# Performance work log

Measured on AMD Instinct MI355X. Metric: run time of the kernel, lower is better.

The kernel has to match this reference:

```python
import jax, jax.numpy as jnp
import numpy as np

B, N, NVT, HS, NZ = 512, 256, 32, 128, 64


def setup_inputs() -> dict:
    key = jax.random.key(0)
    ks = jax.random.split(key, 16)
    node_types = jax.random.randint(ks[0], (B, N), 0, NVT, dtype=jnp.int32)
    node_types = node_types.at[:, 0].set(0)      # START_TYPE
    node_types = node_types.at[:, -1].set(1)     # END_TYPE
    adj = jax.random.randint(ks[1], (B, N, N), 0, 2, dtype=jnp.int32)
    # DAG: edges only u -> v with u < v (strict upper triangular)
    tri = jnp.triu(jnp.ones((N, N), jnp.int32), k=1)
    adj = adj * tri[None, :, :]
    s = 0.05
    p = lambda k, shp: (jax.random.normal(k, shp, jnp.float32) * s)
    return {
        "node_types": node_types,
        "adj": adj,
        "W_ih": p(ks[2], (3 * HS, NVT)),   # grue_forward weight_ih
        "W_hh": p(ks[3], (3 * HS, HS)),    # grue_forward weight_hh
        "b_ih": p(ks[4], (3 * HS,)),
        "b_hh": p(ks[5], (3 * HS,)),
        "Wg": p(ks[6], (HS, NVT)),         # gate_forward linear
        "bg": p(ks[7], (HS,)),
        "Wm": p(ks[8], (HS, NVT)),         # mapper_forward (no bias)
        "W1": p(ks[9], (NZ, HS)),          # fc1 -> mu
        "b1": p(ks[10], (NZ,)),
        "W2": p(ks[11], (NZ, HS)),         # fc2 -> logvar
        "b2": p(ks[12], (NZ,)),
    }


def reference(node_types, adj, W_ih, W_hh, b_ih, b_hh, Wg, bg, Wm, W1, b1, W2, b2):
    hs = Wg.shape[0]
    # one-hot vertex types  [B, N, nvt]
    X = jax.nn.one_hot(node_types, Wg.shape[1], dtype=W_ih.dtype)
    # gated message from each vertex's TYPE (mapper has no bias -> padding contributes 0)
    gated = jax.nn.sigmoid(jnp.einsum('bnv,hv->bnh', X, Wg) + bg) \
            * jnp.einsum('bnv,hv->bnh', X, Wm)                      # [B, N, hs]
    A = adj.astype(gated.dtype)
    # predecessor aggregation: H_v = sum_{u: u->v} gated_u
    Hpre = jnp.einsum('buv,buh->bvh', A, gated)                     # [B, N, hs]
    # torch GRUCell(X_v, Hpre_v), vectorized over all vertices (no recurrence:
    # messages depend only on predecessor types)
    gi = jnp.einsum('bnv,gv->bng', X, W_ih) + b_ih                  # [B, N, 3hs]
    gh = jnp.einsum('bnh,gh->bng', Hpre, W_hh) + b_hh
    r = jax.nn.sigmoid(gi[..., :hs] + gh[..., :hs])
    z = jax.nn.sigmoid(gi[..., hs:2 * hs] + gh[..., hs:2 * hs])
    n = jnp.tanh(gi[..., 2 * hs:] + r * gh[..., 2 * hs:])
    Hv = (1.0 - z) * n + z * Hpre                                   # H_forward, [B, N, hs]
    # graph state: sum over vertices [1, N-1) (start=1, end_offset=1)
    Hg = Hv[:, 1:-1, :].sum(axis=1)                                 # [B, hs]
    mu = Hg @ W1.T + b1
    logvar = Hg @ W2.T + b2
    return (mu, logvar)
```

## Files before the change

### kernel.cpp

```cpp
#include <hip/hip_runtime.h>
#include <hip/hip_bf16.h>

#define HS 128
#define NVT 32
#define NN 256

typedef __attribute__((ext_vector_type(8))) short bf16x8;
typedef __attribute__((ext_vector_type(4))) float f32x4;

#define TABB_OFF 0
#define GIT_OFF  32768

static __device__ __forceinline__ short f2bs(float f) {
    __hip_bfloat16 h = __float2bfloat16(f);
    short s; __builtin_memcpy(&s, &h, 2);
    return s;
}
static __device__ __forceinline__ float bs2f(short s) {
    __hip_bfloat16 h; __builtin_memcpy(&h, &s, 2);
    return __bfloat162float(h);
}
static __device__ __forceinline__ float sigm(float x) {
    return __builtin_amdgcn_rcpf(1.f + __expf(-x));
}

__global__ void __launch_bounds__(512) build_tables(
    const float* __restrict__ W_ih, const float* __restrict__ W_hh,
    const float* __restrict__ b_ih, const float* __restrict__ b_hh,
    const float* __restrict__ Wg,   const float* __restrict__ bg,
    const float* __restrict__ Wm,
    short* __restrict__ TABB, short* __restrict__ GIT)
{
    __shared__ float G_s[HS];
    const int t = blockIdx.x;
    const int j = threadIdx.x;
    if (j < HS) {
        float x = Wg[j * NVT + t] + bg[j];
        G_s[j] = sigm(x) * Wm[j * NVT + t];
    }
    __syncthreads();
    if (j < 384) {
        float acc = 0.f;
        for (int h = 0; h < HS; ++h) acc += G_s[h] * W_hh[j * HS + h];
        TABB[j * NVT + t] = f2bs(acc);
        float git = W_ih[j * NVT + t] + b_ih[j];
        if (j < 256) git += b_hh[j];
        GIT[t * 384 + j] = f2bs(git);
    } else {
        TABB[j * NVT + t] = f2bs(G_s[j - 384]);
    }
}

__global__ void __launch_bounds__(256) dvae_fused(
    const int* __restrict__ node_types, const int* __restrict__ adj,
    const short* __restrict__ TABB, const short* __restrict__ GIT,
    const float* __restrict__ b_hh,
    const float* __restrict__ W1, const float* __restrict__ b1,
    const float* __restrict__ W2, const float* __restrict__ b2,
    float* __restrict__ out)
{
    __shared__ short cntA[NN * 40];
    __shared__ short GITs[NVT * 388];
    __shared__ int   types_s[NN];
    __shared__ float hgp[4 * HS];
    __shared__ float hg_s[HS];

    const int b = blockIdx.x, tid = threadIdx.x;
    const int wave = tid >> 6, lane = tid & 63;
    const int quad = lane >> 4, col = lane & 15;

    types_s[tid] = node_types[b * NN + tid];

    {
        const unsigned* src = (const unsigned*)GIT;
        unsigned* dst = (unsigned*)GITs;
        #pragma unroll
        for (int c = 0; c < 24; ++c) {
            int i = c * 256 + tid;
            int t = i / 192, j = i - t * 192;
            dst[t * 194 + j] = src[i];
        }
    }

    const int* adjb = adj + (size_t)b * NN * NN;
    const int v = tid;
    unsigned c0 = 0, c1 = 0, c2 = 0, c3 = 0, c4 = 0, c5 = 0, c6 = 0, c7 = 0;
    for (int u0 = 0; u0 < NN; u0 += 32) {
        int av[32];
        #pragma unroll
        for (int j = 0; j < 32; ++j) av[j] = adjb[(u0 + j) * NN + v];
        #pragma unroll
        for (int j = 0; j < 32; ++j) {
            unsigned t = (unsigned)__builtin_amdgcn_readfirstlane(types_s[u0 + j]);
            unsigned inc = ((unsigned)av[j]) << ((t & 3u) * 8u);
            switch (t >> 2) {
                case 0: c0 += inc; break;
                case 1: c1 += inc; break;
                case 2: c2 += inc; break;
                case 3: c3 += inc; break;
                case 4: c4 += inc; break;
                case 5: c5 += inc; break;
                case 6: c6 += inc; break;
                default: c7 += inc; break;
            }
        }
    }
    {
        unsigned cc[8] = {c0, c1, c2, c3, c4, c5, c6, c7};
        unsigned* dst = (unsigned*)cntA;
        #pragma unroll
        for (int k = 0; k < 8; ++k) {
            float f0 = (float)(cc[k] & 0xFF),         f1 = (float)((cc[k] >> 8) & 0xFF);
            float f2 = (float)((cc[k] >> 16) & 0xFF), f3 = (float)((cc[k] >> 24) & 0xFF);
            unsigned p0 = (unsigned)(unsigned short)f2bs(f0) | ((unsigned)(unsigned short)f2bs(f1) << 16);
            unsigned p1 = (unsigned)(unsigned short)f2bs(f2) | ((unsigned)(unsigned short)f2bs(f3) << 16);
            dst[v * 20 + 2 * k]     = p0;
            dst[v * 20 + 2 * k + 1] = p1;
        }
    }

    bf16x8 bfrag[8];
    #pragma unroll
    for (int i = 0; i < 8; ++i) {
        int gate = i >> 1, sub = (i & 1) * 16;
        int jb = (gate < 3 ? gate * 128 : 384) + wave * 32 + sub;
        bfrag[i] = *(const bf16x8*)(TABB + (jb + col) * 32 + quad * 8);
    }
    const int h0 = wave * 32 + col;
    const float bhn0 = b_hh[256 + h0], bhn1 = b_hh[256 + h0 + 16];
    float hg0 = 0.f, hg1 = 0.f;
    __syncthreads();

    for (int m = 0; m < 16; ++m) {
        bf16x8 afrag = *(const bf16x8*)(cntA + (m * 16 + col) * 40 + quad * 8);
        f32x4 acc[8];
        #pragma unroll
        for (int i = 0; i < 8; ++i)
            acc[i] = __builtin_amdgcn_mfma_f32_16x16x32_bf16(
                afrag, bfrag[i], (f32x4){0.f, 0.f, 0.f, 0.f}, 0, 0, 0);
        #pragma unroll
        for (int r = 0; r < 4; ++r) {
            int vv = m * 16 + quad * 4 + r;
            int tv = types_s[vv];
            float msk = (vv >= 1 && vv < NN - 1) ? 1.f : 0.f;
            const short* g = GITs + tv * 388;
            {
                float gir = bs2f(g[h0]), giz = bs2f(g[128 + h0]), gin = bs2f(g[256 + h0]);
                float rr = sigm(gir + acc[0][r]);
                float zz = sigm(giz + acc[2][r]);
                float x2 = gin + rr * (acc[4][r] + bhn0);
                float nt = 1.f - 2.f * __builtin_amdgcn_rcpf(1.f + __expf(2.f * x2));
                hg0 += msk * ((1.f - zz) * nt + zz * acc[6][r]);
            }
            {
                int h1 = h0 + 16;
                float gir = bs2f(g[h1]), giz = bs2f(g[128 + h1]), gin = bs2f(g[256 + h1]);
                float rr = sigm(gir + acc[1][r]);
                float zz = sigm(giz + acc[3][r]);
                float x2 = gin + rr * (acc[5][r] + bhn1);
                float nt = 1.f - 2.f * __builtin_amdgcn_rcpf(1.f + __expf(2.f * x2));
                hg1 += msk * ((1.f - zz) * nt + zz * acc[7][r]);
            }
        }
    }

    hgp[quad * HS + h0]      = hg0;
    hgp[quad * HS + h0 + 16] = hg1;
    __syncthreads();
    if (tid < HS)
        hg_s[tid] = (hgp[tid] + hgp[HS + tid]) + (hgp[2 * HS + tid] + hgp[3 * HS + tid]);
    __syncthreads();
    if (tid < 128) {
        int which = tid >> 6, zz = tid & 63;
        const float* W = which ? W2 : W1;
        float acc2 = which ? b2[zz] : b1[zz];
        #pragma unroll 4
        for (int h = 0; h < HS; ++h) acc2 += hg_s[h] * W[zz * HS + h];
        out[which * 32768 + b * 64 + zz] = acc2;
    }
}

extern "C" void kernel_launch(void* const* d_in, const int* in_sizes, int n_in,
                              void* d_out, int out_size, void* d_ws, size_t ws_size,
                              hipStream_t stream)
{
    const int* node_types = (const int*)d_in[0];
    const int* adj        = (const int*)d_in[1];
    const float* W_ih = (const float*)d_in[2];
    const float* W_hh = (const float*)d_in[3];
    const float* b_ih = (const float*)d_in[4];
    const float* b_hh = (const float*)d_in[5];
    const float* Wg   = (const float*)d_in[6];
    const float* bg   = (const float*)d_in[7];
    const float* Wm   = (const float*)d_in[8];
    const float* W1   = (const float*)d_in[9];
    const float* b1   = (const float*)d_in[10];
    const float* W2   = (const float*)d_in[11];
    const float* b2   = (const float*)d_in[12];

    char* ws = (char*)d_ws;
    short* TABB = (short*)(ws + TABB_OFF);
    short* GIT  = (short*)(ws + GIT_OFF);
    float* out  = (float*)d_out;

    build_tables<<<dim3(32), dim3(512), 0, stream>>>(W_ih, W_hh, b_ih, b_hh, Wg, bg, Wm, TABB, GIT);
    dvae_fused<<<dim3(512), dim3(256), 0, stream>>>(node_types, adj, TABB, GIT, b_hh, W1, b1, W2, b2, out);
}
```

Before: 247.8 us.

## Count predecessor types via adjacency bitmasks and popcount, double block to 512 threads

```diff
diff --git a/kernel.cpp b/kernel.cpp
--- a/kernel.cpp
+++ b/kernel.cpp
@@ -51,7 +51,7 @@
     }
 }
 
-__global__ void __launch_bounds__(256) dvae_fused(
+__global__ void __launch_bounds__(512) dvae_fused(
     const int* __restrict__ node_types, const int* __restrict__ adj,
     const short* __restrict__ TABB, const short* __restrict__ GIT,
     const float* __restrict__ b_hh,
@@ -59,123 +59,125 @@
     const float* __restrict__ W2, const float* __restrict__ b2,
     float* __restrict__ out)
 {
-    __shared__ short cntA[NN * 40];
+    __shared__ unsigned cntA[NN * 20];
     __shared__ short GITs[NVT * 388];
-    __shared__ int   types_s[NN];
-    __shared__ float hgp[4 * HS];
+    __shared__ unsigned tmask[NVT * 8];
+    __shared__ int types_s[NN];
     __shared__ float hg_s[HS];
 
     const int b = blockIdx.x, tid = threadIdx.x;
     const int wave = tid >> 6, lane = tid & 63;
     const int quad = lane >> 4, col = lane & 15;
 
-    types_s[tid] = node_types[b * NN + tid];
+    if (tid < NN) types_s[tid] = node_types[b * NN + tid];
 
     {
         const unsigned* src = (const unsigned*)GIT;
         unsigned* dst = (unsigned*)GITs;
         #pragma unroll
-        for (int c = 0; c < 24; ++c) {
-            int i = c * 256 + tid;
+        for (int c = 0; c < 12; ++c) {
+            int i = c * 512 + tid;
             int t = i / 192, j = i - t * 192;
             dst[t * 194 + j] = src[i];
         }
     }
 
-    const int* adjb = adj + (size_t)b * NN * NN;
-    const int v = tid;
-    unsigned c0 = 0, c1 = 0, c2 = 0, c3 = 0, c4 = 0, c5 = 0, c6 = 0, c7 = 0;
-    for (int u0 = 0; u0 < NN; u0 += 32) {
-        int av[32];
-        #pragma unroll
-        for (int j = 0; j < 32; ++j) av[j] = adjb[(u0 + j) * NN + v];
-        #pragma unroll
-        for (int j = 0; j < 32; ++j) {
-            unsigned t = (unsigned)__builtin_amdgcn_readfirstlane(types_s[u0 + j]);
-            unsigned inc = ((unsigned)av[j]) << ((t & 3u) * 8u);
-            switch (t >> 2) {
-                case 0: c0 += inc; break;
-                case 1: c1 += inc; break;
-                case 2: c2 += inc; break;
-                case 3: c3 += inc; break;
-                case 4: c4 += inc; break;
-                case 5: c5 += inc; break;
-                case 6: c6 += inc; break;
-                default: c7 += inc; break;
-            }
-        }
-    }
-    {
-        unsigned cc[8] = {c0, c1, c2, c3, c4, c5, c6, c7};
-        unsigned* dst = (unsigned*)cntA;
-        #pragma unroll
-        for (int k = 0; k < 8; ++k) {
-            float f0 = (float)(cc[k] & 0xFF),         f1 = (float)((cc[k] >> 8) & 0xFF);
-            float f2 = (float)((cc[k] >> 16) & 0xFF), f3 = (float)((cc[k] >> 24) & 0xFF);
-            unsigned p0 = (unsigned)(unsigned short)f2bs(f0) | ((unsigned)(unsigned short)f2bs(f1) << 16);
-            unsigned p1 = (unsigned)(unsigned short)f2bs(f2) | ((unsigned)(unsigned short)f2bs(f3) << 16);
-            dst[v * 20 + 2 * k]     = p0;
-            dst[v * 20 + 2 * k + 1] = p1;
-        }
-    }
-
-    bf16x8 bfrag[8];
+    bf16x8 bfrag[4];
     #pragma unroll
-    for (int i = 0; i < 8; ++i) {
-        int gate = i >> 1, sub = (i & 1) * 16;
-        int jb = (gate < 3 ? gate * 128 : 384) + wave * 32 + sub;
-        bfrag[i] = *(const bf16x8*)(TABB + (jb + col) * 32 + quad * 8);
-    }
-    const int h0 = wave * 32 + col;
-    const float bhn0 = b_hh[256 + h0], bhn1 = b_hh[256 + h0 + 16];
-    float hg0 = 0.f, hg1 = 0.f;
-    __syncthreads();
-
+    for (int g = 0; g < 4; ++g) {
+        int jb = (g < 3 ? g * 128 : 384) + wave * 16;
+        bfrag[g] = *(const bf16x8*)(TABB + (jb + col) * 32 + quad * 8);
+    }
+    const int h0 = wave * 16 + col;
+    const float bhn = b_hh[256 + h0];
+
+    unsigned cb[8];
+    if (tid < NN) {
+        const int* colp = adj + (size_t)b * NN * NN + tid;
+        #pragma unroll
+        for (int w8 = 0; w8 < 8; ++w8) {
+            int avv[32];
+            #pragma unroll
+            for (int j = 0; j < 32; ++j) avv[j] = colp[(w8 * 32 + j) * NN];
+            unsigned wd = 0;
+            #pragma unroll
+            for (int j = 0; j < 32; ++j) wd |= ((unsigned)avv[j]) << j;
+            cb[w8] = wd;
+        }
+    }
+    __syncthreads();
+
+    if (tid < NN) {
+        int t = tid >> 3, w8 = tid & 7;
+        unsigned mw = 0;
+        #pragma unroll
+        for (int k = 0; k < 32; ++k)
+            mw |= ((unsigned)(types_s[w8 * 32 + k] == t)) << k;
+        tmask[tid] = mw;
+    }
+    __syncthreads();
+
+    if (tid < NN) {
+        #pragma unroll
+        for (int tp = 0; tp < 16; ++tp) {
+            const uint4* m0p = (const uint4*)&tmask[(2 * tp) * 8];
+            const uint4* m1p = (const uint4*)&tmask[(2 * tp + 1) * 8];
+            uint4 ma = m0p[0], mb = m0p[1], mc = m1p[0], md = m1p[1];
+            unsigned c0 = __popc(cb[0] & ma.x) + __popc(cb[1] & ma.y)
+                        + __popc(cb[2] & ma.z) + __popc(cb[3] & ma.w)
+                        + __popc(cb[4] & mb.x) + __popc(cb[5] & mb.y)
+                        + __popc(cb[6] & mb.z) + __popc(cb[7] & mb.w);
+            unsigned c1 = __popc(cb[0] & mc.x) + __popc(cb[1] & mc.y)
+                        + __popc(cb[2] & mc.z) + __popc(cb[3] & mc.w)
+                        + __popc(cb[4] & md.x) + __popc(cb[5] & md.y)
+                        + __popc(cb[6] & md.z) + __popc(cb[7] & md.w);
+            unsigned p = (__float_as_uint((float)c0) >> 16)
+                       | (__float_as_uint((float)c1) & 0xFFFF0000u);
+            cntA[tid * 20 + tp] = p;
+        }
+    }
+    __syncthreads();
+
+    float hg = 0.f;
     for (int m = 0; m < 16; ++m) {
-        bf16x8 afrag = *(const bf16x8*)(cntA + (m * 16 + col) * 40 + quad * 8);
-        f32x4 acc[8];
-        #pragma unroll
-        for (int i = 0; i < 8; ++i)
-            acc[i] = __builtin_amdgcn_mfma_f32_16x16x32_bf16(
-                afrag, bfrag[i], (f32x4){0.f, 0.f, 0.f, 0.f}, 0, 0, 0);
+        bf16x8 afrag = *(const bf16x8*)(cntA + (m * 16 + col) * 20 + quad * 4);
+        f32x4 acc[4];
+        #pragma unroll
+        for (int g = 0; g < 4; ++g)
+            acc[g] = __builtin_amdgcn_mfma_f32_16x16x32_bf16(
+                afrag, bfrag[g], (f32x4){0.f, 0.f, 0.f, 0.f}, 0, 0, 0);
         #pragma unroll
         for (int r = 0; r < 4; ++r) {
             int vv = m * 16 + quad * 4 + r;
             int tv = types_s[vv];
+            const short* g = GITs + tv * 388;
+            float gir = bs2f(g[h0]);
+            float giz = bs2f(g[128 + h0]);
+            float gin = bs2f(g[256 + h0]);
+            float rr = sigm(gir + acc[0][r]);
+            float zz = sigm(giz + acc[1][r]);
+            float x2 = gin + rr * (acc[2][r] + bhn);
+            float nt = 1.f - 2.f * __builtin_amdgcn_rcpf(1.f + __expf(2.f * x2));
             float msk = (vv >= 1 && vv < NN - 1) ? 1.f : 0.f;
-            const short* g = GITs + tv * 388;
-            {
-                float gir = bs2f(g[h0]), giz = bs2f(g[128 + h0]), gin = bs2f(g[256 + h0]);
-                float rr = sigm(gir + acc[0][r]);
-                float zz = sigm(giz + acc[2][r]);
-                float x2 = gin + rr * (acc[4][r] + bhn0);
-                float nt = 1.f - 2.f * __builtin_amdgcn_rcpf(1.f + __expf(2.f * x2));
-                hg0 += msk * ((1.f - zz) * nt + zz * acc[6][r]);
-            }
-            {
-                int h1 = h0 + 16;
-                float gir = bs2f(g[h1]), giz = bs2f(g[128 + h1]), gin = bs2f(g[256 + h1]);
-                float rr = sigm(gir + acc[1][r]);
-                float zz = sigm(giz + acc[3][r]);
-                float x2 = gin + rr * (acc[5][r] + bhn1);
-                float nt = 1.f - 2.f * __builtin_amdgcn_rcpf(1.f + __expf(2.f * x2));
-                hg1 += msk * ((1.f - zz) * nt + zz * acc[7][r]);
-            }
-        }
-    }
-
-    hgp[quad * HS + h0]      = hg0;
-    hgp[quad * HS + h0 + 16] = hg1;
-    __syncthreads();
-    if (tid < HS)
-        hg_s[tid] = (hgp[tid] + hgp[HS + tid]) + (hgp[2 * HS + tid] + hgp[3 * HS + tid]);
-    __syncthreads();
+            hg += msk * ((1.f - zz) * nt + zz * acc[3][r]);
+        }
+    }
+    hg += __shfl_xor(hg, 16);
+    hg += __shfl_xor(hg, 32);
+    if (lane < 16) hg_s[h0] = hg;
+    __syncthreads();
+
     if (tid < 128) {
         int which = tid >> 6, zz = tid & 63;
         const float* W = which ? W2 : W1;
         float acc2 = which ? b2[zz] : b1[zz];
-        #pragma unroll 4
-        for (int h = 0; h < HS; ++h) acc2 += hg_s[h] * W[zz * HS + h];
+        const float4* Wv = (const float4*)(W + zz * HS);
+        #pragma unroll
+        for (int i = 0; i < 32; ++i) {
+            float4 ww = Wv[i];
+            acc2 += hg_s[4 * i] * ww.x + hg_s[4 * i + 1] * ww.y
+                  + hg_s[4 * i + 2] * ww.z + hg_s[4 * i + 3] * ww.w;
+        }
         out[which * 32768 + b * 64 + zz] = acc2;
     }
 }
@@ -204,5 +206,5 @@
     float* out  = (float*)d_out;
 
     build_tables<<<dim3(32), dim3(512), 0, stream>>>(W_ih, W_hh, b_ih, b_hh, Wg, bg, Wm, TABB, GIT);
-    dvae_fused<<<dim3(512), dim3(256), 0, stream>>>(node_types, adj, TABB, GIT, b_hh, W1, b1, W2, b2, out);
-}
+    dvae_fused<<<dim3(512), dim3(512), 0, stream>>>(node_types, adj, TABB, GIT, b_hh, W1, b1, W2, b2, out);
+}
```

New measurement: 241.8 us. -2.4%, faster.

## Split adjacency histogram into separate kernel using bitmask popcount over row chunks

Applied to the files above, without the earlier changes.

```diff
diff --git a/kernel.cpp b/kernel.cpp
--- a/kernel.cpp
+++ b/kernel.cpp
@@ -10,6 +10,7 @@
 
 #define TABB_OFF 0
 #define GIT_OFF  32768
+#define CNT8_OFF 65536
 
 static __device__ __forceinline__ short f2bs(float f) {
     __hip_bfloat16 h = __float2bfloat16(f);
@@ -51,18 +52,67 @@
     }
 }
 
-__global__ void __launch_bounds__(256) dvae_fused(
+__global__ void __launch_bounds__(256) hist_part(
     const int* __restrict__ node_types, const int* __restrict__ adj,
+    unsigned char* __restrict__ cnt8)
+{
+    __shared__ unsigned tmask[NVT * 2];
+    const int blk = blockIdx.x;
+    const int b = blk >> 2, c = blk & 3;
+    const int tid = threadIdx.x;
+    const int* adjb = adj + (size_t)b * NN * NN + c * 64 * NN;
+
+    unsigned cb0 = 0, cb1 = 0;
+    {
+        int av[32];
+        #pragma unroll
+        for (int j = 0; j < 32; ++j) av[j] = adjb[j * NN + tid];
+        #pragma unroll
+        for (int j = 0; j < 32; ++j) cb0 |= ((unsigned)av[j]) << j;
+        #pragma unroll
+        for (int j = 0; j < 32; ++j) av[j] = adjb[(32 + j) * NN + tid];
+        #pragma unroll
+        for (int j = 0; j < 32; ++j) cb1 |= ((unsigned)av[j]) << j;
+    }
+    if (tid < 64) {
+        int t = tid >> 1, w2 = tid & 1;
+        const int* ty = node_types + b * NN + c * 64 + w2 * 32;
+        unsigned mw = 0;
+        #pragma unroll
+        for (int k = 0; k < 32; ++k)
+            mw |= ((unsigned)(ty[k] == t)) << k;
+        tmask[tid] = mw;
+    }
+    __syncthreads();
+
+    unsigned outw[8];
+    #pragma unroll
+    for (int q = 0; q < 8; ++q) {
+        unsigned w = 0;
+        #pragma unroll
+        for (int s = 0; s < 4; ++s) {
+            int t = q * 4 + s;
+            unsigned cnt = __popc(cb0 & tmask[2 * t]) + __popc(cb1 & tmask[2 * t + 1]);
+            w |= cnt << (8 * s);
+        }
+        outw[q] = w;
+    }
+    uint4* dst = (uint4*)(cnt8 + ((size_t)blk * NN + tid) * 32);
+    dst[0] = make_uint4(outw[0], outw[1], outw[2], outw[3]);
+    dst[1] = make_uint4(outw[4], outw[5], outw[6], outw[7]);
+}
+
+__global__ void __launch_bounds__(256) dvae_main(
+    const int* __restrict__ node_types, const unsigned char* __restrict__ cnt8,
     const short* __restrict__ TABB, const short* __restrict__ GIT,
     const float* __restrict__ b_hh,
     const float* __restrict__ W1, const float* __restrict__ b1,
     const float* __restrict__ W2, const float* __restrict__ b2,
     float* __restrict__ out)
 {
-    __shared__ short cntA[NN * 40];
+    __shared__ unsigned cntA[NN * 20];
     __shared__ short GITs[NVT * 388];
-    __shared__ int   types_s[NN];
-    __shared__ float hgp[4 * HS];
+    __shared__ int types_s[NN];
     __shared__ float hg_s[HS];
 
     const int b = blockIdx.x, tid = threadIdx.x;
@@ -70,6 +120,30 @@
     const int quad = lane >> 4, col = lane & 15;
 
     types_s[tid] = node_types[b * NN + tid];
+
+    {
+        uint4 a0, a1;
+        {
+            const uint4* s = (const uint4*)(cnt8 + ((size_t)(b * 4 + 0) * NN + tid) * 32);
+            a0 = s[0]; a1 = s[1];
+        }
+        #pragma unroll
+        for (int c = 1; c < 4; ++c) {
+            const uint4* s = (const uint4*)(cnt8 + ((size_t)(b * 4 + c) * NN + tid) * 32);
+            uint4 p0 = s[0], p1 = s[1];
+            a0.x += p0.x; a0.y += p0.y; a0.z += p0.z; a0.w += p0.w;
+            a1.x += p1.x; a1.y += p1.y; a1.z += p1.z; a1.w += p1.w;
+        }
+        unsigned acc8[8] = {a0.x, a0.y, a0.z, a0.w, a1.x, a1.y, a1.z, a1.w};
+        #pragma unroll
+        for (int q = 0; q < 8; ++q) {
+            unsigned u = acc8[q];
+            float f0 = (float)(u & 0xFF),         f1 = (float)((u >> 8) & 0xFF);
+            float f2 = (float)((u >> 16) & 0xFF), f3 = (float)((u >> 24) & 0xFF);
+            cntA[tid * 20 + 2 * q]     = (__float_as_uint(f0) >> 16) | (__float_as_uint(f1) & 0xFFFF0000u);
+            cntA[tid * 20 + 2 * q + 1] = (__float_as_uint(f2) >> 16) | (__float_as_uint(f3) & 0xFFFF0000u);
+        }
+    }
 
     {
         const unsigned* src = (const unsigned*)GIT;
@@ -79,43 +153,6 @@
             int i = c * 256 + tid;
             int t = i / 192, j = i - t * 192;
             dst[t * 194 + j] = src[i];
-        }
-    }
-
-    const int* adjb = adj + (size_t)b * NN * NN;
-    const int v = tid;
-    unsigned c0 = 0, c1 = 0, c2 = 0, c3 = 0, c4 = 0, c5 = 0, c6 = 0, c7 = 0;
-    for (int u0 = 0; u0 < NN; u0 += 32) {
-        int av[32];
-        #pragma unroll
-        for (int j = 0; j < 32; ++j) av[j] = adjb[(u0 + j) * NN + v];
-        #pragma unroll
-        for (int j = 0; j < 32; ++j) {
-            unsigned t = (unsigned)__builtin_amdgcn_readfirstlane(types_s[u0 + j]);
-            unsigned inc = ((unsigned)av[j]) << ((t & 3u) * 8u);
-            switch (t >> 2) {
-                case 0: c0 += inc; break;
-                case 1: c1 += inc; break;
-                case 2: c2 += inc; break;
-                case 3: c3 += inc; break;
-                case 4: c4 += inc; break;
-                case 5: c5 += inc; break;
-                case 6: c6 += inc; break;
-                default: c7 += inc; break;
-            }
-        }
-    }
-    {
-        unsigned cc[8] = {c0, c1, c2, c3, c4, c5, c6, c7};
-        unsigned* dst = (unsigned*)cntA;
-        #pragma unroll
-        for (int k = 0; k < 8; ++k) {
-            float f0 = (float)(cc[k] & 0xFF),         f1 = (float)((cc[k] >> 8) & 0xFF);
-            float f2 = (float)((cc[k] >> 16) & 0xFF), f3 = (float)((cc[k] >> 24) & 0xFF);
-            unsigned p0 = (unsigned)(unsigned short)f2bs(f0) | ((unsigned)(unsigned short)f2bs(f1) << 16);
-            unsigned p1 = (unsigned)(unsigned short)f2bs(f2) | ((unsigned)(unsigned short)f2bs(f3) << 16);
-            dst[v * 20 + 2 * k]     = p0;
-            dst[v * 20 + 2 * k + 1] = p1;
         }
     }
 
@@ -132,7 +169,7 @@
     __syncthreads();
 
     for (int m = 0; m < 16; ++m) {
-        bf16x8 afrag = *(const bf16x8*)(cntA + (m * 16 + col) * 40 + quad * 8);
+        bf16x8 afrag = *(const bf16x8*)(cntA + (m * 16 + col) * 20 + quad * 4);
         f32x4 acc[8];
         #pragma unroll
         for (int i = 0; i < 8; ++i)
@@ -145,37 +182,38 @@
             float msk = (vv >= 1 && vv < NN - 1) ? 1.f : 0.f;
             const short* g = GITs + tv * 388;
             {
-                float gir = bs2f(g[h0]), giz = bs2f(g[128 + h0]), gin = bs2f(g[256 + h0]);
-                float rr = sigm(gir + acc[0][r]);
-                float zz = sigm(giz + acc[2][r]);
-                float x2 = gin + rr * (acc[4][r] + bhn0);
+                float rr = sigm(bs2f(g[h0]) + acc[0][r]);
+                float zz = sigm(bs2f(g[128 + h0]) + acc[2][r]);
+                float x2 = bs2f(g[256 + h0]) + rr * (acc[4][r] + bhn0);
                 float nt = 1.f - 2.f * __builtin_amdgcn_rcpf(1.f + __expf(2.f * x2));
                 hg0 += msk * ((1.f - zz) * nt + zz * acc[6][r]);
             }
             {
                 int h1 = h0 + 16;
-                float gir = bs2f(g[h1]), giz = bs2f(g[128 + h1]), gin = bs2f(g[256 + h1]);
-                float rr = sigm(gir + acc[1][r]);
-                float zz = sigm(giz + acc[3][r]);
-                float x2 = gin + rr * (acc[5][r] + bhn1);
+                float rr = sigm(bs2f(g[h1]) + acc[1][r]);
+                float zz = sigm(bs2f(g[128 + h1]) + acc[3][r]);
+                float x2 = bs2f(g[256 + h1]) + rr * (acc[5][r] + bhn1);
                 float nt = 1.f - 2.f * __builtin_amdgcn_rcpf(1.f + __expf(2.f * x2));
                 hg1 += msk * ((1.f - zz) * nt + zz * acc[7][r]);
             }
         }
     }
-
-    hgp[quad * HS + h0]      = hg0;
-    hgp[quad * HS + h0 + 16] = hg1;
-    __syncthreads();
-    if (tid < HS)
-        hg_s[tid] = (hgp[tid] + hgp[HS + tid]) + (hgp[2 * HS + tid] + hgp[3 * HS + tid]);
-    __syncthreads();
+    hg0 += __shfl_xor(hg0, 16); hg0 += __shfl_xor(hg0, 32);
+    hg1 += __shfl_xor(hg1, 16); hg1 += __shfl_xor(hg1, 32);
+    if (lane < 16) { hg_s[h0] = hg0; hg_s[h0 + 16] = hg1; }
+    __syncthreads();
+
     if (tid < 128) {
         int which = tid >> 6, zz = tid & 63;
         const float* W = which ? W2 : W1;
         float acc2 = which ? b2[zz] : b1[zz];
-        #pragma unroll 4
-        for (int h = 0; h < HS; ++h) acc2 += hg_s[h] * W[zz * HS + h];
+        const float4* Wv = (const float4*)(W + zz * HS);
+        #pragma unroll
+        for (int i = 0; i < 32; ++i) {
+            float4 ww = Wv[i];
+            acc2 += hg_s[4 * i] * ww.x + hg_s[4 * i + 1] * ww.y
+                  + hg_s[4 * i + 2] * ww.z + hg_s[4 * i + 3] * ww.w;
+        }
         out[which * 32768 + b * 64 + zz] = acc2;
     }
 }
@@ -201,8 +239,10 @@
     char* ws = (char*)d_ws;
     short* TABB = (short*)(ws + TABB_OFF);
     short* GIT  = (short*)(ws + GIT_OFF);
+    unsigned char* cnt8 = (unsigned char*)(ws + CNT8_OFF);
     float* out  = (float*)d_out;
 
     build_tables<<<dim3(32), dim3(512), 0, stream>>>(W_ih, W_hh, b_ih, b_hh, Wg, bg, Wm, TABB, GIT);
-    dvae_fused<<<dim3(512), dim3(256), 0, stream>>>(node_types, adj, TABB, GIT, b_hh, W1, b1, W2, b2, out);
-}
+    hist_part<<<dim3(2048), dim3(256), 0, stream>>>(node_types, adj, cnt8);
+    dvae_main<<<dim3(512), dim3(256), 0, stream>>>(node_types, cnt8, TABB, GIT, b_hh, W1, b1, W2, b2, out);
+}
```

New measurement: 254.4 us. 2.7% more time.
